# Optimization experiments

Hardware: AMD Instinct MI355X
Metric: run time of the kernel (lower is better)

Reference implementation:

```python
import jax, jax.numpy as jnp
import numpy as np

D = 1024
H = 8          # MHA fallback num_heads
DH = D // H
DFF = 4096     # mlp_ratio * hidden_size
EPS = 1e-6


def _ln(x, g, b):
    mu = jnp.mean(x, axis=-1, keepdims=True)
    var = jnp.mean((x - mu) ** 2, axis=-1, keepdims=True)
    return (x - mu) * jax.lax.rsqrt(var + EPS) * g + b


def setup_inputs() -> dict:
    key = jax.random.key(0)
    ks = jax.random.split(key, 16)
    s = 0.02
    return {
        "x": jax.random.normal(ks[0], (8, 1024, D), jnp.float32),
        "c": jax.random.normal(ks[1], (8, D), jnp.float32),
        # Mamba-block (attention fallback) params
        "m_ada_w": jax.random.normal(ks[2], (D, 3 * D), jnp.float32) * s,
        "m_ada_b": jnp.zeros((3 * D,), jnp.float32),
        "m_norm_g": jnp.ones((D,), jnp.float32),
        "m_norm_b": jnp.zeros((D,), jnp.float32),
        "in_proj_w": jax.random.normal(ks[3], (3 * D, D), jnp.float32) * s,
        "in_proj_b": jnp.zeros((3 * D,), jnp.float32),
        "out_proj_w": jax.random.normal(ks[4], (D, D), jnp.float32) * s,
        "out_proj_b": jnp.zeros((D,), jnp.float32),
        # FeedForward-block params
        "f_ada_w": jax.random.normal(ks[5], (D, 3 * D), jnp.float32) * s,
        "f_ada_b": jnp.zeros((3 * D,), jnp.float32),
        "f_norm_g": jnp.ones((D,), jnp.float32),
        "f_norm_b": jnp.zeros((D,), jnp.float32),
        "w1": jax.random.normal(ks[6], (D, DFF), jnp.float32) * s,
        "b1": jnp.zeros((DFF,), jnp.float32),
        "w2": jax.random.normal(ks[7], (DFF, D), jnp.float32) * s,
        "b2": jnp.zeros((D,), jnp.float32),
    }


def reference(x, c, m_ada_w, m_ada_b, m_norm_g, m_norm_b, in_proj_w, in_proj_b,
              out_proj_w, out_proj_b, f_ada_w, f_ada_b, f_norm_g, f_norm_b,
              w1, b1, w2, b2):
    B, N, _ = x.shape
    # ---- MambaBlock (MHA fallback), dropout = identity (eval) ----
    mod = jax.nn.silu(c) @ m_ada_w + m_ada_b              # (B, 3D)
    shift, scale, gate = jnp.split(mod, 3, axis=-1)
    h = _ln(x, m_norm_g, m_norm_b)
    h = h * (1.0 + scale[:, None, :]) + shift[:, None, :]
    qkv = h @ in_proj_w.T + in_proj_b                      # (B, N, 3D)
    q, k, v = jnp.split(qkv, 3, axis=-1)
    q = q.reshape(B, N, H, DH)
    k = k.reshape(B, N, H, DH)
    v = v.reshape(B, N, H, DH)
    scores = jnp.einsum("bqhd,bkhd->bhqk", q, k) / np.sqrt(DH).astype(np.float32)
    attn = jax.nn.softmax(scores, axis=-1)
    o = jnp.einsum("bhqk,bkhd->bqhd", attn, v).reshape(B, N, D)
    o = o @ out_proj_w.T + out_proj_b
    x = x + gate[:, None, :] * o
    # ---- FeedForward block ----
    mod2 = jax.nn.silu(c) @ f_ada_w + f_ada_b
    shift2, scale2, gate2 = jnp.split(mod2, 3, axis=-1)
    h = _ln(x, f_norm_g, f_norm_b)
    h = h * (1.0 + scale2[:, None, :]) + shift2[:, None, :]
    h = jax.nn.gelu(h @ w1 + b1, approximate=False) @ w2 + b2
    return x + gate2[:, None, :] * h
```

## Files before the change

kernel.cpp:

```cpp
#include <hip/hip_runtime.h>

typedef __bf16 bf16x8 __attribute__((ext_vector_type(8)));
typedef float f32x4 __attribute__((ext_vector_type(4)));

__device__ __forceinline__ unsigned short f2bf(float f) {
    unsigned int u = __float_as_uint(f);
    unsigned int r = (u + 0x7FFFu + ((u >> 16) & 1u)) >> 16;
    return (unsigned short)r;
}

__device__ __forceinline__ void gload16(const void* g, void* l) {
    __builtin_amdgcn_global_load_lds(
        (const __attribute__((address_space(1))) unsigned int*)g,
        (__attribute__((address_space(3))) unsigned int*)l, 16, 0, 0);
}

__device__ __forceinline__ void barrier_raw() {
    asm volatile("" ::: "memory");
    __builtin_amdgcn_s_barrier();
    asm volatile("" ::: "memory");
}

__device__ __forceinline__ void vmwait0() {
    asm volatile("s_waitcnt vmcnt(0)" ::: "memory");
}

__device__ __forceinline__ float gelu_fast(float u) {
    float z = 1.595769122f * u + 0.071354816f * u * u * u;
    return u / (1.f + __expf(-z));
}

__global__ __launch_bounds__(256) void f2b4(const float* __restrict__ in,
                                            unsigned short* __restrict__ out) {
    size_t i = ((size_t)blockIdx.x * 256 + threadIdx.x) * 4;
    float4 v = *(const float4*)(in + i);
    ushort4 o;
    o.x = f2bf(v.x); o.y = f2bf(v.y); o.z = f2bf(v.z); o.w = f2bf(v.w);
    *(ushort4*)(out + i) = o;
}

__global__ __launch_bounds__(256) void transpose_f2b(const float* __restrict__ in,
                                                     unsigned short* __restrict__ out,
                                                     int R, int C) {
    __shared__ float tile[32][33];
    int r0 = blockIdx.y * 32, c0 = blockIdx.x * 32;
    int tx = threadIdx.x & 31, ty = threadIdx.x >> 5;
#pragma unroll
    for (int i = 0; i < 4; i++) {
        int r = ty + i * 8;
        tile[r][tx] = in[(size_t)(r0 + r) * C + c0 + tx];
    }
    __syncthreads();
#pragma unroll
    for (int i = 0; i < 4; i++) {
        int r = ty + i * 8;
        out[(size_t)(c0 + r) * R + r0 + tx] = f2bf(tile[tx][r]);
    }
}

__global__ __launch_bounds__(256) void ada_mod_part(const float* __restrict__ c,
                                                    const float* __restrict__ W,
                                                    float* __restrict__ partial) {
    __shared__ float sc[8 * 64];
    int kc = blockIdx.y * 64;
    for (int i = threadIdx.x; i < 512; i += 256) {
        int b = i >> 6, k = i & 63;
        float cv = c[b * 1024 + kc + k];
        sc[i] = cv / (1.f + __expf(-cv));
    }
    __syncthreads();
    int j = blockIdx.x * 256 + threadIdx.x;
    float acc[8] = {0, 0, 0, 0, 0, 0, 0, 0};
    for (int k = 0; k < 64; k++) {
        float w = W[(size_t)(kc + k) * 3072 + j];
#pragma unroll
        for (int b = 0; b < 8; b++) acc[b] += sc[b * 64 + k] * w;
    }
#pragma unroll
    for (int b = 0; b < 8; b++) partial[((size_t)blockIdx.y * 8 + b) * 3072 + j] = acc[b];
}

__global__ __launch_bounds__(256) void ada_reduce(const float* __restrict__ partial,
                                                  const float* __restrict__ bias,
                                                  float* __restrict__ out) {
    int idx = blockIdx.x * 256 + threadIdx.x;
    int b = idx / 3072;
    int jj = idx - b * 3072;
    float s = bias[jj];
#pragma unroll
    for (int ch = 0; ch < 16; ch++) s += partial[((size_t)ch * 8 + b) * 3072 + jj];
    out[idx] = s;
}

__global__ __launch_bounds__(256) void ln_mod_kernel(const float* __restrict__ x,
                                                     const float* __restrict__ gamma,
                                                     const float* __restrict__ beta,
                                                     const float* __restrict__ mods,
                                                     unsigned short* __restrict__ out) {
    int row = blockIdx.x;
    int b = row >> 10;
    float4 v = ((const float4*)(x + (size_t)row * 1024))[threadIdx.x];
    float s = v.x + v.y + v.z + v.w;
    float s2 = v.x * v.x + v.y * v.y + v.z * v.z + v.w * v.w;
#pragma unroll
    for (int d = 1; d < 64; d <<= 1) { s += __shfl_xor(s, d); s2 += __shfl_xor(s2, d); }
    __shared__ float red[8];
    int lane = threadIdx.x & 63, wid = threadIdx.x >> 6;
    if (lane == 0) { red[wid] = s; red[4 + wid] = s2; }
    __syncthreads();
    float S = red[0] + red[1] + red[2] + red[3];
    float S2 = red[4] + red[5] + red[6] + red[7];
    float mu = S * (1.f / 1024.f);
    float var = S2 * (1.f / 1024.f) - mu * mu;
    float rs = rsqrtf(var + 1e-6f);
    const float* mrow = mods + b * 3072;
    int j0 = threadIdx.x * 4;
    float hv[4] = {v.x, v.y, v.z, v.w};
    ushort4 o;
    unsigned short* op = (unsigned short*)&o;
#pragma unroll
    for (int i = 0; i < 4; i++) {
        int j = j0 + i;
        float hh = (hv[i] - mu) * rs * gamma[j] + beta[j];
        hh = hh * (1.f + mrow[1024 + j]) + mrow[j];
        op[i] = f2bf(hh);
    }
    *(ushort4*)(out + (size_t)row * 1024 + j0) = o;
}

template <int EP>
__global__ __launch_bounds__(256, 2) void gemmw(const unsigned short* __restrict__ A,
                                                const unsigned short* __restrict__ Bt,
                                                int N, int K, int ny,
                                                const float* __restrict__ bias,
                                                unsigned short* __restrict__ outb,
                                                unsigned short* __restrict__ vt) {
    constexpr int AE = 128 * 32;
    constexpr int BE = 256 * 32;
    extern __shared__ __align__(16) char smem[];
    __bf16* As = (__bf16*)smem;
    __bf16* Bs = As + 2 * AE;

    int tid = threadIdx.x, lane = tid & 63, wid = tid >> 6;
    int t = lane & 15, g = lane >> 4;
    int xk2 = ((t >> 1) & 3) * 8;

    int nwg = gridDim.x, chunk = nwg >> 3;
    int swz = (blockIdx.x & 7) * chunk + (blockIdx.x >> 3);
    int bx = swz / ny, by = swz % ny;
    int rowA0 = by * 128, colB0 = bx * 256;

    int rin = tid >> 2, cblk = tid & 3;
    int scol = (cblk ^ ((rin >> 1) & 3)) * 8;

    auto stage = [&](int nb, int kt) {
        int k0 = kt << 5;
        gload16(A + (size_t)(rowA0 + rin) * K + k0 + scol, As + nb * AE + tid * 8);
        gload16(A + (size_t)(rowA0 + 64 + rin) * K + k0 + scol,
                As + nb * AE + 2048 + tid * 8);
#pragma unroll
        for (int sl = 0; sl < 4; sl++)
            gload16(Bt + (size_t)(colB0 + sl * 64 + rin) * K + k0 + scol,
                    Bs + nb * BE + sl * 2048 + tid * 8);
    };

    f32x4 acc[8][4];
#pragma unroll
    for (int m = 0; m < 8; m++)
#pragma unroll
        for (int n = 0; n < 4; n++) acc[m][n] = (f32x4){0.f, 0.f, 0.f, 0.f};

    stage(0, 0);
    vmwait0();
    barrier_raw();

    int NT = K >> 5;
#pragma unroll 2
    for (int kt = 0; kt < NT; ++kt) {
        const __bf16* Ac = As + (kt & 1) * AE;
        const __bf16* Bc = Bs + (kt & 1) * BE;
        bool more = (kt + 1) < NT;
        if (more) stage((kt & 1) ^ 1, kt + 1);

        bf16x8 b[4];
#pragma unroll
        for (int n = 0; n < 4; n++)
            b[n] = *(const bf16x8*)&Bc[(wid * 64 + n * 16 + t) * 32 + ((g * 8) ^ xk2)];

        __builtin_amdgcn_s_setprio(1);
#pragma unroll
        for (int mh = 0; mh < 2; mh++) {
            bf16x8 a[4];
#pragma unroll
            for (int m4 = 0; m4 < 4; m4++)
                a[m4] = *(const bf16x8*)&Ac[(mh * 64 + m4 * 16 + t) * 32 + ((g * 8) ^ xk2)];
#pragma unroll
            for (int m4 = 0; m4 < 4; m4++)
#pragma unroll
                for (int n = 0; n < 4; n++)
                    acc[mh * 4 + m4][n] =
                        __builtin_amdgcn_mfma_f32_16x16x32_bf16(a[m4], b[n], acc[mh * 4 + m4][n], 0, 0, 0);
        }
        __builtin_amdgcn_s_setprio(0);

        if (more) {
            vmwait0();
            barrier_raw();
        }
    }

    int col0 = colB0 + wid * 64;
    bool vpart = (EP == 0) && (colB0 >= 2048);
#pragma unroll
    for (int m = 0; m < 8; m++)
#pragma unroll
        for (int n = 0; n < 4; n++) {
            int col = col0 + n * 16 + t;
            if (EP == 0 && vpart) {
                int hcol = col - 2048;
                int hh = hcol >> 7, d = hcol & 127;
                int bb = rowA0 >> 10;
                int ntok = (rowA0 + m * 16 + g * 4) & 1023;
                float bs = bias[col];
                ushort4 vv;
                vv.x = f2bf(acc[m][n][0] + bs);
                vv.y = f2bf(acc[m][n][1] + bs);
                vv.z = f2bf(acc[m][n][2] + bs);
                vv.w = f2bf(acc[m][n][3] + bs);
                *(ushort4*)(vt + (((size_t)(bb * 8 + hh) * 128 + d) * 1024 + ntok)) = vv;
            } else {
#pragma unroll
                for (int r = 0; r < 4; r++) {
                    int row = rowA0 + m * 16 + g * 4 + r;
                    float v = acc[m][n][r];
                    if (EP == 0) {
                        outb[(size_t)row * N + col] = f2bf(v + bias[col]);
                    } else {
                        outb[(size_t)row * N + col] = f2bf(gelu_fast(v + bias[col]));
                    }
                }
            }
        }
}

template <int EP>
__global__ __launch_bounds__(256, 4) void gemmo(const unsigned short* __restrict__ A,
                                                const unsigned short* __restrict__ Bt,
                                                int N, int K, int nx,
                                                const float* __restrict__ bias,
                                                const float* __restrict__ xres,
                                                const float* __restrict__ mods,
                                                float* __restrict__ outf) {
    constexpr int AE = 128 * 32;
    constexpr int BE = 128 * 32;
    extern __shared__ __align__(16) char smem[];
    __bf16* As = (__bf16*)smem;
    __bf16* Bs = As + 2 * AE;

    int tid = threadIdx.x, lane = tid & 63, wid = tid >> 6;
    int wr = wid >> 1, wc = wid & 1;
    int t = lane & 15, g = lane >> 4;
    int xk2 = ((t >> 1) & 3) * 8;

    int nwg = gridDim.x, chunk = nwg >> 3;
    int swz = (blockIdx.x & 7) * chunk + (blockIdx.x >> 3);
    int bx = swz % nx, by = swz / nx;
    int rowA0 = by * 128, colB0 = bx * 128;

    int rin = tid >> 2, cblk = tid & 3;
    int scol = (cblk ^ ((rin >> 1) & 3)) * 8;

    auto stage = [&](int nb, int kt) {
        int k0 = kt << 5;
        gload16(A + (size_t)(rowA0 + rin) * K + k0 + scol, As + nb * AE + tid * 8);
        gload16(A + (size_t)(rowA0 + 64 + rin) * K + k0 + scol,
                As + nb * AE + 2048 + tid * 8);
        gload16(Bt + (size_t)(colB0 + rin) * K + k0 + scol, Bs + nb * BE + tid * 8);
        gload16(Bt + (size_t)(colB0 + 64 + rin) * K + k0 + scol,
                Bs + nb * BE + 2048 + tid * 8);
    };

    f32x4 acc[4][4];
#pragma unroll
    for (int m = 0; m < 4; m++)
#pragma unroll
        for (int n = 0; n < 4; n++) acc[m][n] = (f32x4){0.f, 0.f, 0.f, 0.f};

    stage(0, 0);
    vmwait0();
    barrier_raw();

    int NT = K >> 5;
#pragma unroll 2
    for (int kt = 0; kt < NT; ++kt) {
        const __bf16* Ac = As + (kt & 1) * AE;
        const __bf16* Bc = Bs + (kt & 1) * BE;
        bool more = (kt + 1) < NT;
        if (more) stage((kt & 1) ^ 1, kt + 1);

        bf16x8 a[4], b[4];
#pragma unroll
        for (int m = 0; m < 4; m++)
            a[m] = *(const bf16x8*)&Ac[(wr * 64 + m * 16 + t) * 32 + ((g * 8) ^ xk2)];
#pragma unroll
        for (int n = 0; n < 4; n++)
            b[n] = *(const bf16x8*)&Bc[(wc * 64 + n * 16 + t) * 32 + ((g * 8) ^ xk2)];

        __builtin_amdgcn_s_setprio(1);
#pragma unroll
        for (int m = 0; m < 4; m++)
#pragma unroll
            for (int n = 0; n < 4; n++)
                acc[m][n] = __builtin_amdgcn_mfma_f32_16x16x32_bf16(a[m], b[n], acc[m][n], 0, 0, 0);
        __builtin_amdgcn_s_setprio(0);

        if (more) {
            vmwait0();
            barrier_raw();
        }
    }

    int row0 = rowA0 + wr * 64, col0 = colB0 + wc * 64;
#pragma unroll
    for (int m = 0; m < 4; m++)
#pragma unroll
        for (int n = 0; n < 4; n++) {
            int col = col0 + n * 16 + t;
#pragma unroll
            for (int r = 0; r < 4; r++) {
                int row = row0 + m * 16 + g * 4 + r;
                float v = acc[m][n][r];
                int bb = row >> 10;
                float gt = mods[bb * 3072 + 2048 + col];
                if (EP == 1) {
                    outf[(size_t)row * 1024 + col] =
                        xres[(size_t)row * 1024 + col] + gt * (v + bias[col]);
                } else {
                    outf[(size_t)row * 1024 + col] += gt * (v + bias[col]);
                }
            }
        }
}

__global__ __launch_bounds__(512, 4) void attn_kernel(const unsigned short* __restrict__ qkv,
                                                      const unsigned short* __restrict__ vt,
                                                      unsigned short* __restrict__ o) {
    extern __shared__ __align__(16) char asmem[];
    __bf16* Ks = (__bf16*)asmem;
    __bf16* Vts = Ks + 2 * 64 * 128;

    int bid = blockIdx.x;
    int logical = (bid & 7) * 64 + (bid >> 3);
    int q0 = (logical & 7) * 128;
    int bh = logical >> 3;
    int b = bh >> 3, h = bh & 7;
    int tid = threadIdx.x, lane = tid & 63, w = tid >> 6;
    int t = lane & 15, g = lane >> 4;
    int swzt = (t & 7) << 4;

    const unsigned short* qbase = qkv + (size_t)(b * 1024) * 3072 + h * 128;
    int qrow = q0 + w * 16 + t;
    bf16x8 qf[4];
#pragma unroll
    for (int ks = 0; ks < 4; ks++)
        qf[ks] = *(const bf16x8*)(qbase + (size_t)qrow * 3072 + ks * 32 + g * 8);

    f32x4 Oa[8];
#pragma unroll
    for (int n = 0; n < 8; n++) Oa[n] = (f32x4){0.f, 0.f, 0.f, 0.f};
    float m_r = -1e30f, l_r = 0.f;
    const float scale = 0.08838834764831845f;

    int krow = tid >> 4;
    int ksrc = (((tid & 15) * 16) ^ ((krow & 7) << 4)) >> 1;
    int vrow = tid >> 3;
    int vsrc = (((tid & 7) * 16) ^ ((vrow & 7) << 4)) >> 1;
    const unsigned short* vtg = vt + (size_t)bh * 128 * 1024;

    auto stage = [&](int buf, int kv0) {
        const unsigned short* kb = qkv + (size_t)(b * 1024 + kv0) * 3072 + 1024 + h * 128;
#pragma unroll
        for (int cc = 0; cc < 2; cc++) {
            gload16(kb + (size_t)(cc * 32 + krow) * 3072 + ksrc,
                    (void*)(Ks + buf * 8192 + cc * 4096 + tid * 8));
            gload16(vtg + (size_t)(cc * 64 + vrow) * 1024 + kv0 + vsrc,
                    (void*)(Vts + buf * 8192 + cc * 4096 + tid * 8));
        }
    };

    stage(0, 0);
    vmwait0();
    barrier_raw();

#pragma unroll 1
    for (int tile = 0; tile < 16; ++tile) {
        int cur = tile & 1;
        bool more = tile < 15;
        if (more) stage(cur ^ 1, (tile + 1) * 64);
        const __bf16* Kc = Ks + cur * 8192;
        const __bf16* Vc = Vts + cur * 8192;

        f32x4 St[4];
#pragma unroll
        for (int n = 0; n < 4; n++) St[n] = (f32x4){0.f, 0.f, 0.f, 0.f};
        __builtin_amdgcn_s_setprio(1);
#pragma unroll
        for (int ks = 0; ks < 4; ks++) {
#pragma unroll
            for (int n = 0; n < 4; n++) {
                bf16x8 kf = *(const bf16x8*)&Kc[(n * 16 + t) * 128 + (((ks * 64 + g * 16) ^ swzt) >> 1)];
                St[n] = __builtin_amdgcn_mfma_f32_16x16x32_bf16(kf, qf[ks], St[n], 0, 0, 0);
            }
        }
        __builtin_amdgcn_s_setprio(0);

        float mx = -1e30f;
#pragma unroll
        for (int n = 0; n < 4; n++)
#pragma unroll
            for (int r = 0; r < 4; r++) mx = fmaxf(mx, St[n][r]);
        mx *= scale;
        mx = fmaxf(mx, __shfl_xor(mx, 16));
        mx = fmaxf(mx, __shfl_xor(mx, 32));
        float mn = fmaxf(m_r, mx);
        float alpha = __expf(m_r - mn);
        m_r = mn;
        float p[4][4];
        float rs = 0.f;
#pragma unroll
        for (int n = 0; n < 4; n++)
#pragma unroll
            for (int r = 0; r < 4; r++) {
                float pv = __expf(St[n][r] * scale - mn);
                p[n][r] = pv;
                rs += pv;
            }
        rs += __shfl_xor(rs, 16);
        rs += __shfl_xor(rs, 32);
        l_r = l_r * alpha + rs;

        unsigned P01[4], P23[4];
#pragma unroll
        for (int n = 0; n < 4; n++) {
            P01[n] = (unsigned)f2bf(p[n][0]) | ((unsigned)f2bf(p[n][1]) << 16);
            P23[n] = (unsigned)f2bf(p[n][2]) | ((unsigned)f2bf(p[n][3]) << 16);
        }

#pragma unroll
        for (int r = 0; r < 4; r++) {
            float ar = __shfl(alpha, (lane & 48) + g * 4 + r);
#pragma unroll
            for (int n2 = 0; n2 < 8; n2++) Oa[n2][r] *= ar;
        }

#pragma unroll
        for (int ks2 = 0; ks2 < 2; ks2++) {
            int e = ks2 * 2, od = ks2 * 2 + 1;
            unsigned s16a = (g < 2) ? P01[e] : P01[od];
            unsigned s16b = (g < 2) ? P23[e] : P23[od];
            unsigned s32a = (g & 1) ? P01[e] : P01[od];
            unsigned s32b = (g & 1) ? P23[e] : P23[od];
            unsigned s48a = (g >= 2) ? P01[e] : P01[od];
            unsigned s48b = (g >= 2) ? P23[e] : P23[od];
            unsigned r16a = __shfl_xor(s16a, 16), r16b = __shfl_xor(s16b, 16);
            unsigned r32a = __shfl_xor(s32a, 32), r32b = __shfl_xor(s32b, 32);
            unsigned r48a = __shfl_xor(s48a, 48), r48b = __shfl_xor(s48b, 48);
            union { unsigned u[4]; bf16x8 v; } pa;
            pa.u[0] = (g == 0) ? P01[e] : (g == 1) ? r48a : (g == 2) ? r32a : r16a;
            pa.u[1] = (g == 0) ? P23[e] : (g == 1) ? r48b : (g == 2) ? r32b : r16b;
            pa.u[2] = (g == 0) ? r16a : (g == 1) ? r32a : (g == 2) ? r48a : P01[od];
            pa.u[3] = (g == 0) ? r16b : (g == 1) ? r32b : (g == 2) ? r48b : P23[od];
            __builtin_amdgcn_s_setprio(1);
#pragma unroll
            for (int n2 = 0; n2 < 8; n2++) {
                bf16x8 vf = *(const bf16x8*)&Vc[(n2 * 16 + t) * 64 + (((ks2 * 64 + g * 16) ^ swzt) >> 1)];
                Oa[n2] = __builtin_amdgcn_mfma_f32_16x16x32_bf16(pa.v, vf, Oa[n2], 0, 0, 0);
            }
            __builtin_amdgcn_s_setprio(0);
        }

        if (more) {
            vmwait0();
            barrier_raw();
        }
    }

#pragma unroll
    for (int r = 0; r < 4; r++) {
        float lq = __shfl(l_r, (lane & 48) + g * 4 + r);
        float inv = 1.f / lq;
        int orow = q0 + w * 16 + g * 4 + r;
#pragma unroll
        for (int n2 = 0; n2 < 8; n2++)
            o[(size_t)(b * 1024 + orow) * 1024 + h * 128 + n2 * 16 + t] = f2bf(Oa[n2][r] * inv);
    }
}

extern "C" void kernel_launch(void* const* d_in, const int* in_sizes, int n_in,
                              void* d_out, int out_size, void* d_ws, size_t ws_size,
                              hipStream_t stream) {
    const float* x          = (const float*)d_in[0];
    const float* c          = (const float*)d_in[1];
    const float* m_ada_w    = (const float*)d_in[2];
    const float* m_ada_b    = (const float*)d_in[3];
    const float* m_norm_g   = (const float*)d_in[4];
    const float* m_norm_b   = (const float*)d_in[5];
    const float* in_proj_w  = (const float*)d_in[6];
    const float* in_proj_b  = (const float*)d_in[7];
    const float* out_proj_w = (const float*)d_in[8];
    const float* out_proj_b = (const float*)d_in[9];
    const float* f_ada_w    = (const float*)d_in[10];
    const float* f_ada_b    = (const float*)d_in[11];
    const float* f_norm_g   = (const float*)d_in[12];
    const float* f_norm_b   = (const float*)d_in[13];
    const float* w1         = (const float*)d_in[14];
    const float* b1         = (const float*)d_in[15];
    const float* w2         = (const float*)d_in[16];
    const float* b2         = (const float*)d_in[17];
    float* out = (float*)d_out;
    char* ws = (char*)d_ws;

    unsigned short* Wq   = (unsigned short*)(ws + 0);
    unsigned short* Wo   = (unsigned short*)(ws + 6291456);
    unsigned short* vt   = (unsigned short*)(ws + 8388608);
    unsigned short* W1t  = (unsigned short*)(ws + 8388608);
    unsigned short* W2t  = (unsigned short*)(ws + 16777216);
    float*          modm = (float*)(ws + 25165824);
    float*          modf = (float*)(ws + 25264128);
    unsigned short* hbuf = (unsigned short*)(ws + 25362432);
    float*          part = (float*)(ws + 25362432);
    float*          part2= (float*)(ws + 25362432 + 2097152);
    unsigned short* qkv  = (unsigned short*)(ws + 42139648);
    unsigned short* obuf = (unsigned short*)(ws + 92471296);
    unsigned short* h2   = (unsigned short*)(ws + 42139648);

    hipFuncSetAttribute((const void*)&gemmw<0>, hipFuncAttributeMaxDynamicSharedMemorySize, 49152);
    hipFuncSetAttribute((const void*)&gemmw<2>, hipFuncAttributeMaxDynamicSharedMemorySize, 49152);
    hipFuncSetAttribute((const void*)&gemmo<1>, hipFuncAttributeMaxDynamicSharedMemorySize, 32768);
    hipFuncSetAttribute((const void*)&gemmo<3>, hipFuncAttributeMaxDynamicSharedMemorySize, 32768);
    hipFuncSetAttribute((const void*)&attn_kernel, hipFuncAttributeMaxDynamicSharedMemorySize, 65536);

    hipLaunchKernelGGL(ada_mod_part, dim3(12, 16), dim3(256), 0, stream, c, m_ada_w, part);
    hipLaunchKernelGGL(ada_mod_part, dim3(12, 16), dim3(256), 0, stream, c, f_ada_w, part2);
    hipLaunchKernelGGL(ada_reduce, dim3(96), dim3(256), 0, stream, part, m_ada_b, modm);
    hipLaunchKernelGGL(ada_reduce, dim3(96), dim3(256), 0, stream, part2, f_ada_b, modf);

    hipLaunchKernelGGL(f2b4, dim3(3072), dim3(256), 0, stream, in_proj_w, Wq);
    hipLaunchKernelGGL(f2b4, dim3(1024), dim3(256), 0, stream, out_proj_w, Wo);

    hipLaunchKernelGGL(ln_mod_kernel, dim3(8192), dim3(256), 0, stream, x, m_norm_g, m_norm_b, modm, hbuf);
    hipLaunchKernelGGL(HIP_KERNEL_NAME(gemmw<0>), dim3(768), dim3(256), 49152, stream,
                       hbuf, Wq, 3072, 1024, 64, in_proj_b, qkv, vt);
    hipLaunchKernelGGL(attn_kernel, dim3(512), dim3(512), 65536, stream, qkv, vt, obuf);
    hipLaunchKernelGGL(HIP_KERNEL_NAME(gemmo<1>), dim3(512), dim3(256), 32768, stream,
                       obuf, Wo, 1024, 1024, 8, out_proj_b, x, modm, out);

    hipLaunchKernelGGL(transpose_f2b, dim3(128, 32), dim3(256), 0, stream, w1, W1t, 1024, 4096);
    hipLaunchKernelGGL(transpose_f2b, dim3(32, 128), dim3(256), 0, stream, w2, W2t, 4096, 1024);

    hipLaunchKernelGGL(ln_mod_kernel, dim3(8192), dim3(256), 0, stream, out, f_norm_g, f_norm_b, modf, hbuf);
    hipLaunchKernelGGL(HIP_KERNEL_NAME(gemmw<2>), dim3(1024), dim3(256), 49152, stream,
                       hbuf, W1t, 4096, 1024, 64, b1, h2, (unsigned short*)nullptr);
    hipLaunchKernelGGL(HIP_KERNEL_NAME(gemmo<3>), dim3(512), dim3(256), 32768, stream,
                       h2, W2t, 1024, 4096, 8, b2, (const float*)nullptr, modf, out);
}
```

Before: 394.2 us.

## Triple-buffer GEMM shared-memory staging and switch wide GEMM to column-major tile order

Both GEMM kernels move from double to triple buffering of the A/B tiles in LDS. Loads are issued two k-steps ahead and the wait is a partial vmcnt instead of a full drain, to hide more global-load latency behind the MFMA work. The wide GEMM also changes its block-to-tile mapping from row-fastest to column-fastest, which alters L2 reuse. The LDS footprint grows by half (72KB and 48KB), which can reduce how many workgroups fit on each CU.

Measured after the change: 386.6 us. Within noise of the previous version (-1.9%).

```diff
diff --git a/kernel.cpp b/kernel.cpp
--- a/kernel.cpp
+++ b/kernel.cpp
@@ -131,7 +131,7 @@
 template <int EP>
 __global__ __launch_bounds__(256, 2) void gemmw(const unsigned short* __restrict__ A,
                                                 const unsigned short* __restrict__ Bt,
-                                                int N, int K, int ny,
+                                                int N, int K, int nx,
                                                 const float* __restrict__ bias,
                                                 unsigned short* __restrict__ outb,
                                                 unsigned short* __restrict__ vt) {
@@ -139,7 +139,7 @@
     constexpr int BE = 256 * 32;
     extern __shared__ __align__(16) char smem[];
     __bf16* As = (__bf16*)smem;
-    __bf16* Bs = As + 2 * AE;
+    __bf16* Bs = As + 3 * AE;
 
     int tid = threadIdx.x, lane = tid & 63, wid = tid >> 6;
     int t = lane & 15, g = lane >> 4;
@@ -147,7 +147,7 @@
 
     int nwg = gridDim.x, chunk = nwg >> 3;
     int swz = (blockIdx.x & 7) * chunk + (blockIdx.x >> 3);
-    int bx = swz / ny, by = swz % ny;
+    int bx = swz % nx, by = swz / nx;
     int rowA0 = by * 128, colB0 = bx * 256;
 
     int rin = tid >> 2, cblk = tid & 3;
@@ -170,17 +170,24 @@
 #pragma unroll
         for (int n = 0; n < 4; n++) acc[m][n] = (f32x4){0.f, 0.f, 0.f, 0.f};
 
+    int NT = K >> 5;
     stage(0, 0);
-    vmwait0();
+    if (NT > 1) {
+        stage(1, 1);
+        asm volatile("s_waitcnt vmcnt(6)" ::: "memory");
+    } else {
+        vmwait0();
+    }
     barrier_raw();
 
-    int NT = K >> 5;
-#pragma unroll 2
+    int cur = 0, tgt = 2;
+#pragma unroll 1
     for (int kt = 0; kt < NT; ++kt) {
-        const __bf16* Ac = As + (kt & 1) * AE;
-        const __bf16* Bc = Bs + (kt & 1) * BE;
+        bool deep = (kt + 2) < NT;
         bool more = (kt + 1) < NT;
-        if (more) stage((kt & 1) ^ 1, kt + 1);
+        if (deep) stage(tgt, kt + 2);
+        const __bf16* Ac = As + cur * AE;
+        const __bf16* Bc = Bs + cur * BE;
 
         bf16x8 b[4];
 #pragma unroll
@@ -204,9 +211,15 @@
         __builtin_amdgcn_s_setprio(0);
 
         if (more) {
-            vmwait0();
+            if (deep) {
+                asm volatile("s_waitcnt vmcnt(6)" ::: "memory");
+            } else {
+                vmwait0();
+            }
             barrier_raw();
         }
+        cur = (cur == 2) ? 0 : cur + 1;
+        tgt = (tgt == 2) ? 0 : tgt + 1;
     }
 
     int col0 = colB0 + wid * 64;
@@ -255,7 +268,7 @@
     constexpr int BE = 128 * 32;
     extern __shared__ __align__(16) char smem[];
     __bf16* As = (__bf16*)smem;
-    __bf16* Bs = As + 2 * AE;
+    __bf16* Bs = As + 3 * AE;
 
     int tid = threadIdx.x, lane = tid & 63, wid = tid >> 6;
     int wr = wid >> 1, wc = wid & 1;
@@ -286,17 +299,24 @@
 #pragma unroll
         for (int n = 0; n < 4; n++) acc[m][n] = (f32x4){0.f, 0.f, 0.f, 0.f};
 
+    int NT = K >> 5;
     stage(0, 0);
-    vmwait0();
+    if (NT > 1) {
+        stage(1, 1);
+        asm volatile("s_waitcnt vmcnt(4)" ::: "memory");
+    } else {
+        vmwait0();
+    }
     barrier_raw();
 
-    int NT = K >> 5;
-#pragma unroll 2
+    int cur = 0, tgt = 2;
+#pragma unroll 1
     for (int kt = 0; kt < NT; ++kt) {
-        const __bf16* Ac = As + (kt & 1) * AE;
-        const __bf16* Bc = Bs + (kt & 1) * BE;
+        bool deep = (kt + 2) < NT;
         bool more = (kt + 1) < NT;
-        if (more) stage((kt & 1) ^ 1, kt + 1);
+        if (deep) stage(tgt, kt + 2);
+        const __bf16* Ac = As + cur * AE;
+        const __bf16* Bc = Bs + cur * BE;
 
         bf16x8 a[4], b[4];
 #pragma unroll
@@ -315,9 +335,15 @@
         __builtin_amdgcn_s_setprio(0);
 
         if (more) {
-            vmwait0();
+            if (deep) {
+                asm volatile("s_waitcnt vmcnt(4)" ::: "memory");
+            } else {
+                vmwait0();
+            }
             barrier_raw();
         }
+        cur = (cur == 2) ? 0 : cur + 1;
+        tgt = (tgt == 2) ? 0 : tgt + 1;
     }
 
     int row0 = rowA0 + wr * 64, col0 = colB0 + wc * 64;
@@ -534,10 +560,10 @@
     unsigned short* obuf = (unsigned short*)(ws + 92471296);
     unsigned short* h2   = (unsigned short*)(ws + 42139648);
 
-    hipFuncSetAttribute((const void*)&gemmw<0>, hipFuncAttributeMaxDynamicSharedMemorySize, 49152);
-    hipFuncSetAttribute((const void*)&gemmw<2>, hipFuncAttributeMaxDynamicSharedMemorySize, 49152);
-    hipFuncSetAttribute((const void*)&gemmo<1>, hipFuncAttributeMaxDynamicSharedMemorySize, 32768);
-    hipFuncSetAttribute((const void*)&gemmo<3>, hipFuncAttributeMaxDynamicSharedMemorySize, 32768);
+    hipFuncSetAttribute((const void*)&gemmw<0>, hipFuncAttributeMaxDynamicSharedMemorySize, 73728);
+    hipFuncSetAttribute((const void*)&gemmw<2>, hipFuncAttributeMaxDynamicSharedMemorySize, 73728);
+    hipFuncSetAttribute((const void*)&gemmo<1>, hipFuncAttributeMaxDynamicSharedMemorySize, 49152);
+    hipFuncSetAttribute((const void*)&gemmo<3>, hipFuncAttributeMaxDynamicSharedMemorySize, 49152);
     hipFuncSetAttribute((const void*)&attn_kernel, hipFuncAttributeMaxDynamicSharedMemorySize, 65536);
 
     hipLaunchKernelGGL(ada_mod_part, dim3(12, 16), dim3(256), 0, stream, c, m_ada_w, part);
@@ -549,18 +575,18 @@
     hipLaunchKernelGGL(f2b4, dim3(1024), dim3(256), 0, stream, out_proj_w, Wo);
 
     hipLaunchKernelGGL(ln_mod_kernel, dim3(8192), dim3(256), 0, stream, x, m_norm_g, m_norm_b, modm, hbuf);
-    hipLaunchKernelGGL(HIP_KERNEL_NAME(gemmw<0>), dim3(768), dim3(256), 49152, stream,
-                       hbuf, Wq, 3072, 1024, 64, in_proj_b, qkv, vt);
+    hipLaunchKernelGGL(HIP_KERNEL_NAME(gemmw<0>), dim3(768), dim3(256), 73728, stream,
+                       hbuf, Wq, 3072, 1024, 12, in_proj_b, qkv, vt);
     hipLaunchKernelGGL(attn_kernel, dim3(512), dim3(512), 65536, stream, qkv, vt, obuf);
-    hipLaunchKernelGGL(HIP_KERNEL_NAME(gemmo<1>), dim3(512), dim3(256), 32768, stream,
+    hipLaunchKernelGGL(HIP_KERNEL_NAME(gemmo<1>), dim3(512), dim3(256), 49152, stream,
                        obuf, Wo, 1024, 1024, 8, out_proj_b, x, modm, out);
 
     hipLaunchKernelGGL(transpose_f2b, dim3(128, 32), dim3(256), 0, stream, w1, W1t, 1024, 4096);
     hipLaunchKernelGGL(transpose_f2b, dim3(32, 128), dim3(256), 0, stream, w2, W2t, 4096, 1024);
 
     hipLaunchKernelGGL(ln_mod_kernel, dim3(8192), dim3(256), 0, stream, out, f_norm_g, f_norm_b, modf, hbuf);
-    hipLaunchKernelGGL(HIP_KERNEL_NAME(gemmw<2>), dim3(1024), dim3(256), 49152, stream,
-                       hbuf, W1t, 4096, 1024, 64, b1, h2, (unsigned short*)nullptr);
-    hipLaunchKernelGGL(HIP_KERNEL_NAME(gemmo<3>), dim3(512), dim3(256), 32768, stream,
+    hipLaunchKernelGGL(HIP_KERNEL_NAME(gemmw<2>), dim3(1024), dim3(256), 73728, stream,
+                       hbuf, W1t, 4096, 1024, 16, b1, h2, (unsigned short*)nullptr);
+    hipLaunchKernelGGL(HIP_KERNEL_NAME(gemmo<3>), dim3(512), dim3(256), 49152, stream,
                        h2, W2t, 1024, 4096, 8, b2, (const float*)nullptr, modf, out);
 }
```
